# Optimization experiments

Hardware: AMD Instinct MI355X
Metric: run time of the kernel (lower is better)

Reference implementation:

```python
import jax, jax.numpy as jnp
import numpy as np

F_DIM = 4096
HID = 256
COR = 32
N_FRAMES = 200
NB = 30
TS = 9  # 4 + 5 time_steps


def _gru(xg, hg, wx, wh, bx, bh):
    # torch.nn.GRU cell math, gates ordered (r, z, n)
    gx = xg @ wx + bx
    gh = hg @ wh + bh
    xr, xz, xn = jnp.split(gx, 3, axis=-1)
    hr, hz, hn = jnp.split(gh, 3, axis=-1)
    r = jax.nn.sigmoid(xr + hr)
    z = jax.nn.sigmoid(xz + hz)
    n = jnp.tanh(xn + r * hn)
    return (1.0 - z) * n + z * hg


def _sattn(h, mask):
    # parameter-free scaled dot-product attention across active tracks
    d = jnp.asarray(h.shape[-1], h.dtype)
    s = (h @ h.T) / jnp.sqrt(d)
    s = jnp.where(mask[None, :], s, -1e9)
    a = jax.nn.softmax(s, axis=-1)
    out = a @ h
    return jnp.where(mask[:, None], out, h)


def setup_inputs() -> dict:
    key = jax.random.key(0)
    ks = jax.random.split(key, 20)
    flow = jax.random.normal(ks[0], (1, N_FRAMES, NB + 1, F_DIM), jnp.float32)
    x = jax.random.normal(ks[1], (1, N_FRAMES, NB + 1, F_DIM), jnp.float32)
    # y: [track_id, x1,y1,x2,y2, label, conf, d0..d5] -> 13 channels
    track = jnp.broadcast_to(jnp.arange(1, NB + 1, dtype=jnp.float32)[None, None, :, None], (1, N_FRAMES, NB, 1))
    coords = jax.random.uniform(ks[2], (1, N_FRAMES, NB, 4), jnp.float32, 0.0, 1000.0)
    label = jnp.round(jax.random.uniform(ks[3], (1, N_FRAMES, NB, 1), jnp.float32))
    conf = jax.random.uniform(ks[4], (1, N_FRAMES, NB, 1), jnp.float32)
    dist = jax.random.normal(ks[5], (1, N_FRAMES, NB, 6), jnp.float32)
    y = jnp.concatenate([track, coords, label, conf, dist], axis=-1)
    toa = jnp.ones((1, 1), jnp.float32)
    s = 0.02
    p = lambda k, shp: s * jax.random.normal(k, shp, jnp.float32)
    return {
        "x": x, "y": y, "toa": toa, "flow": flow,
        "W_rgb": p(ks[6], (F_DIM, HID)), "b_rgb": jnp.zeros((HID,), jnp.float32),
        "W_bb": p(ks[7], (5, HID)), "b_bb": jnp.zeros((HID,), jnp.float32),
        "W_dd": p(ks[8], (6, HID)), "b_dd": jnp.zeros((HID,), jnp.float32),
        "W_proj": p(ks[9], (HID, COR)), "b_proj": jnp.zeros((COR,), jnp.float32),
        "Wx_c": p(ks[10], (COR, 3 * COR)), "Wh_c": p(ks[11], (COR, 3 * COR)),
        "bx_c": jnp.zeros((3 * COR,), jnp.float32), "bh_c": jnp.zeros((3 * COR,), jnp.float32),
        "Wx_g": p(ks[12], (2 * HID, 3 * HID)), "Wh_g": p(ks[13], (HID, 3 * HID)),
        "bx_g": jnp.zeros((3 * HID,), jnp.float32), "bh_g": jnp.zeros((3 * HID,), jnp.float32),
        "W_out": p(ks[14], (2 * HID + COR, 1)), "b_out": jnp.zeros((1,), jnp.float32),
        "W_pbox": p(ks[15], (2 * HID + COR, 4 * TS)), "b_pbox": jnp.zeros((4 * TS,), jnp.float32),
    }


def reference(x, y, toa, flow, W_rgb, b_rgb, W_bb, b_bb, W_dd, b_dd, W_proj, b_proj,
              Wx_c, Wh_c, bx_c, bh_c, Wx_g, Wh_g, bx_g, bh_g, W_out, b_out, W_pbox, b_pbox):
    T = x.shape[1] - TS
    norm = jnp.array([1920.0, 1200.0, 1920.0, 1200.0], y.dtype)
    nb = y[0, :, :, 1:5] / norm                      # (N, 30, 4) normalized boxes
    # future targets: 9 future frames of normalized boxes, flattened -> (T, 30, 36)
    fut = jnp.concatenate([nb[1 + i:1 + i + T] for i in range(TS)], axis=-1)
    flow_f = flow[0, :T]                             # (T, 31, F)
    yf = y[0, :T]                                    # (T, 30, 13)
    nbf = nb[:T]
    act = yf[..., 0] != 0                            # (T, 30) active-track mask

    def step(carry, inp):
        h, hc, bacc, oacc = carry
        ft, yt, nbt, futt, at = inp
        atf = at.astype(h.dtype)
        rgb = jax.nn.relu(ft @ W_rgb + b_rgb)        # (31, H)
        img = jnp.broadcast_to(rgb[0], (NB, rgb.shape[-1]))
        comb = jnp.concatenate([rgb[1:], img], axis=-1)            # (30, 2H)
        bfeat = jax.nn.relu(jnp.concatenate([nbt, yt[:, 6:7]], axis=-1) @ W_bb + b_bb)
        dfeat = jax.nn.relu(yt[:, 7:13] @ W_dd + b_dd)
        xc = dfeat @ W_proj + b_proj
        hc_n = _gru(xc, hc, Wx_c, Wh_c, bx_c, bh_c)  # CorGRU, output_cor = hidden
        h_n = _gru(comb, h, Wx_g, Wh_g, bx_g, bh_g)
        feat = jnp.concatenate([h_n, bfeat, hc_n], axis=-1)        # (30, 2H+32)
        logit = (feat @ W_out + b_out)[:, 0]
        pbox = feat @ W_pbox + b_pbox                # (30, 36)
        d = pbox - futt
        ad = jnp.abs(d)
        sl1 = jnp.mean(jnp.where(ad < 1.0, 0.5 * d * d, ad - 0.5), axis=-1)  # SmoothL1 per box
        bacc = bacc + jnp.sum(sl1 * atf)
        tgt = yt[:, 5]
        bce = jnp.maximum(logit, 0.0) - logit * tgt + jnp.log1p(jnp.exp(-jnp.abs(logit)))
        oacc = oacc + 0.05 * jnp.sum(bce * atf)
        h2 = jnp.where(at[:, None], h_n, h)
        hc2 = jnp.where(at[:, None], hc_n, hc)
        return (_sattn(h2, at), _sattn(hc2, at), bacc, oacc), None

    init = (jnp.zeros((NB, HID), flow.dtype), jnp.zeros((NB, COR), flow.dtype),
            jnp.zeros((), flow.dtype), jnp.zeros((), flow.dtype))
    (h, hc, bbox_l, obj_l), _ = jax.lax.scan(step, init, (flow_f, yf, nbf, fut, act))
    total = obj_l + bbox_l + 0.3 * bbox_l            # object + bbox + inter(0.3*bbox)
    return total
```

## Files before the change

kernel.cpp:

```cpp
#include <hip/hip_runtime.h>
#include <hip/hip_bf16.h>
#include <math.h>
#include <stdint.h>

#define T_STEPS 191
#define NB1 31
#define YS 13

__device__ __forceinline__ float sigmoid_(float x) { return 1.f / (1.f + expf(-x)); }
__device__ __forceinline__ float bflo(unsigned u) { return __uint_as_float(u << 16); }
__device__ __forceinline__ float bfhi(unsigned u) { return __uint_as_float(u & 0xffff0000u); }

__device__ __forceinline__ void store_dw_mall(float* p, float v) {
    asm volatile("global_store_dword %0, %1, off sc0 sc1"
                 :: "v"((uintptr_t)p), "v"(v) : "memory");
}
__device__ __forceinline__ void atomic_inc_mall(unsigned* p) {
    asm volatile("global_atomic_add %0, %1, off sc1"
                 :: "v"((uintptr_t)p), "v"(1u) : "memory");
}
__device__ __forceinline__ unsigned load_u32_mall(const unsigned* p) {
    unsigned v;
    asm volatile("global_load_dword %0, %1, off sc0 sc1\n\ts_waitcnt vmcnt(0)"
                 : "=v"(v) : "v"((uintptr_t)p) : "memory");
    return v;
}

template <bool GATHER, bool RELU>
__global__ __launch_bounds__(256) void gemm_tiled(
    const float* __restrict__ A, const float* __restrict__ B,
    const float* __restrict__ bias, float* __restrict__ C,
    int M, int N, int K)
{
    __shared__ float As[16][65];
    __shared__ float Bs[16][65];
    const int tid = threadIdx.x;
    const int tm = tid >> 4, tn = tid & 15;
    const int rowBase = blockIdx.y * 64;
    const int colBase = blockIdx.x * 64;
    float acc[4][4] = {};
    for (int kt = 0; kt < K; kt += 16) {
        #pragma unroll
        for (int l = 0; l < 4; ++l) {
            const int idx = tid + l * 256;
            const int kk = idx & 15, rr = idx >> 4;
            const int row = rowBase + rr;
            float v = 0.f;
            if (row < M) {
                if (GATHER) {
                    const int t = row / 30, i = row - t * 30;
                    const int k = kt + kk;
                    const int src = (k < 256) ? ((t * NB1 + i + 1) * 256 + k)
                                              : (t * NB1 * 256 + (k - 256));
                    v = A[src];
                } else {
                    v = A[(size_t)row * K + kt + kk];
                }
            }
            As[kk][rr] = v;
            const int nn = idx & 63, k2 = idx >> 6;
            Bs[k2][nn] = B[(size_t)(kt + k2) * N + colBase + nn];
        }
        __syncthreads();
        #pragma unroll
        for (int kk = 0; kk < 16; ++kk) {
            float a[4], b[4];
            #pragma unroll
            for (int i = 0; i < 4; ++i) a[i] = As[kk][tm * 4 + i];
            #pragma unroll
            for (int j = 0; j < 4; ++j) b[j] = Bs[kk][tn * 4 + j];
            #pragma unroll
            for (int i = 0; i < 4; ++i)
                #pragma unroll
                for (int j = 0; j < 4; ++j)
                    acc[i][j] = fmaf(a[i], b[j], acc[i][j]);
        }
        __syncthreads();
    }
    #pragma unroll
    for (int i = 0; i < 4; ++i) {
        const int row = rowBase + tm * 4 + i;
        if (row < M) {
            #pragma unroll
            for (int j = 0; j < 4; ++j) {
                const int col = colBase + tn * 4 + j;
                float v = acc[i][j] + bias[col];
                if (RELU) v = fmaxf(v, 0.f);
                C[(size_t)row * N + col] = v;
            }
        }
    }
}

__global__ __launch_bounds__(256) void prep_w(const float* __restrict__ Whg, unsigned* __restrict__ wp)
{
    const int idx = blockIdx.x * 256 + threadIdx.x;
    if (idx >= 128 * 768) return;
    const int k2 = idx / 768, c = idx - k2 * 768;
    __hip_bfloat16 b0 = __float2bfloat16(Whg[(size_t)(2 * k2) * 768 + c]);
    __hip_bfloat16 b1 = __float2bfloat16(Whg[(size_t)(2 * k2 + 1) * 768 + c]);
    const unsigned lo = *reinterpret_cast<unsigned short*>(&b0);
    const unsigned hi = *reinterpret_cast<unsigned short*>(&b1);
    wp[idx] = lo | (hi << 16);
}

__global__ void prep_bias(const float* __restrict__ bxg, const float* __restrict__ bhg,
                          const float* __restrict__ bxc, const float* __restrict__ bhc,
                          float* __restrict__ biasg, float* __restrict__ biasc)
{
    const int t = threadIdx.x;
    if (t < 768) biasg[t] = bxg[t] + (t < 512 ? bhg[t] : 0.f);
    if (t < 96)  biasc[t] = bxc[t] + (t < 64 ? bhc[t] : 0.f);
}

__global__ __launch_bounds__(256) void precomp_kernel(
    const float* __restrict__ y,
    const float* __restrict__ Wbb, const float* __restrict__ bbb,
    const float* __restrict__ Wdd, const float* __restrict__ bdd,
    const float* __restrict__ Wproj, const float* __restrict__ bproj,
    const float* __restrict__ Wxc, const float* __restrict__ biasc,
    const float* __restrict__ Wpbox, const float* __restrict__ bpbox,
    const float* __restrict__ Wout, const float* __restrict__ bout,
    float* __restrict__ gxc, float* __restrict__ pbox_b, float* __restrict__ logit_b)
{
    const int m = blockIdx.x;
    const int tid = threadIdx.x;
    __shared__ float bf[256], df[256], xcs[32], yl[16];
    if (tid < YS) yl[tid] = y[m * YS + tid];
    __syncthreads();
    const float invnorm[4] = {1.f/1920.f, 1.f/1200.f, 1.f/1920.f, 1.f/1200.f};
    {
        float s = bbb[tid];
        s = fmaf(yl[1] * invnorm[0], Wbb[0 * 256 + tid], s);
        s = fmaf(yl[2] * invnorm[1], Wbb[1 * 256 + tid], s);
        s = fmaf(yl[3] * invnorm[2], Wbb[2 * 256 + tid], s);
        s = fmaf(yl[4] * invnorm[3], Wbb[3 * 256 + tid], s);
        s = fmaf(yl[6],              Wbb[4 * 256 + tid], s);
        bf[tid] = fmaxf(s, 0.f);
    }
    {
        float s = bdd[tid];
        #pragma unroll
        for (int k = 0; k < 6; ++k) s = fmaf(yl[7 + k], Wdd[k * 256 + tid], s);
        df[tid] = fmaxf(s, 0.f);
    }
    __syncthreads();
    {
        const int c = tid >> 3, p = tid & 7;
        float s = 0.f;
        for (int k = p; k < 256; k += 8) s = fmaf(df[k], Wproj[k * 32 + c], s);
        s += __shfl_xor(s, 1); s += __shfl_xor(s, 2); s += __shfl_xor(s, 4);
        if (p == 0) xcs[c] = s + bproj[c];
    }
    __syncthreads();
    if (tid < 96) {
        float s = biasc[tid];
        #pragma unroll
        for (int k = 0; k < 32; ++k) s = fmaf(xcs[k], Wxc[k * 96 + tid], s);
        gxc[m * 96 + tid] = s;
    }
    {
        const int d = tid >> 2, p = tid & 3;
        if (d < 37) {
            float s = 0.f;
            if (d < 36) {
                for (int k = p; k < 256; k += 4) s = fmaf(bf[k], Wpbox[(256 + k) * 36 + d], s);
            } else {
                for (int k = p; k < 256; k += 4) s = fmaf(bf[k], Wout[256 + k], s);
            }
            s += __shfl_xor(s, 1); s += __shfl_xor(s, 2);
            if (p == 0) {
                if (d < 36) pbox_b[m * 36 + d] = s + bpbox[d];
                else        logit_b[m] = s + bout[0];
            }
        }
    }
}

__device__ __forceinline__ void softmax30(const float* s, float* w) {
    float mx = -INFINITY;
    for (int j = 0; j < 30; ++j) mx = fmaxf(mx, s[j]);
    float sum = 0.f;
    for (int j = 0; j < 30; ++j) { const float e = expf(s[j] - mx); w[j] = e; sum += e; }
    const float inv = 1.f / sum;
    for (int j = 0; j < 30; ++j) w[j] *= inv;
}

#define PH 260
#define PC 36

__global__ __launch_bounds__(768) void seq_kernel(
    const float* __restrict__ y,
    const float* __restrict__ gxg,
    const float* __restrict__ gxc,
    const float* __restrict__ pbox_b,
    const float* __restrict__ logit_b,
    const unsigned* __restrict__ wp,
    const float* __restrict__ bhg,
    const float* __restrict__ Whc,
    const float* __restrict__ bhc,
    const float* __restrict__ Wpbox,
    const float* __restrict__ Wout,
    float* __restrict__ h2buf,
    float* __restrict__ hc2buf,
    unsigned* __restrict__ bar,
    float* __restrict__ partials)
{
    const int r = blockIdx.x;
    const int tid = threadIdx.x;
    __shared__ __align__(16) float h[256];
    __shared__ float gat[768];
    __shared__ float hn[256];
    __shared__ __align__(16) float h2l[256];
    __shared__ float hcs[32], hcg[96], hcn[32];
    __shared__ __align__(16) float hc2l[32];
    __shared__ float whc[32 * 96];
    __shared__ float sc[32], sc2[32], attw[32], attw2[32], pbl[40];
    __shared__ __align__(16) float h2s[30 * PH];
    __shared__ __align__(16) float hc2s[30 * PC];

    for (int i = tid; i < 32 * 96; i += 768) whc[i] = Whc[i];
    if (tid < 256) h[tid] = 0.f;
    if (tid < 32) hcs[tid] = 0.f;
    __syncthreads();

    float bacc = 0.f, oacc = 0.f;

    for (int t = 0; t < T_STEPS; ++t) {
        const int m = t * 30 + r;
        const bool act = (y[m * YS] != 0.f);
        const float actf = act ? 1.f : 0.f;
        const int buf = t & 1;
        float* hb  = h2buf  + buf * (30 * 256);
        float* hcb = hc2buf + buf * (30 * 32);

        {
            const unsigned* wc = wp + tid;
            const float4* h4 = (const float4*)h;
            float acc = 0.f;
            #pragma unroll 8
            for (int k2 = 0; k2 < 128; k2 += 2) {
                const float4 hv = h4[k2 >> 1];
                const unsigned w0 = wc[(size_t)k2 * 768];
                const unsigned w1 = wc[(size_t)(k2 + 1) * 768];
                acc = fmaf(hv.x, bflo(w0), acc);
                acc = fmaf(hv.y, bfhi(w0), acc);
                acc = fmaf(hv.z, bflo(w1), acc);
                acc = fmaf(hv.w, bfhi(w1), acc);
            }
            gat[tid] = acc + (tid < 512 ? gxg[(size_t)m * 768 + tid] : bhg[tid]);
        }
        if (tid < 96) {
            float a = (tid < 64) ? gxc[m * 96 + tid] : bhc[tid];
            #pragma unroll
            for (int k = 0; k < 32; ++k) a = fmaf(hcs[k], whc[k * 96 + tid], a);
            hcg[tid] = a;
        }
        __syncthreads();

        if (tid < 256) {
            const float rg = sigmoid_(gat[tid]);
            const float zg = sigmoid_(gat[256 + tid]);
            const float xn = gxg[(size_t)m * 768 + 512 + tid];
            const float ng = tanhf(xn + rg * gat[512 + tid]);
            const float hv = h[tid];
            const float hnv = (1.f - zg) * ng + zg * hv;
            hn[tid] = hnv;
            const float h2v = act ? hnv : hv;
            h2l[tid] = h2v;
            store_dw_mall(hb + r * 256 + tid, h2v);
        } else if (tid < 288) {
            const int j = tid - 256;
            const float rg = sigmoid_(hcg[j]);
            const float zg = sigmoid_(hcg[32 + j]);
            const float xn = gxc[m * 96 + 64 + j];
            const float ng = tanhf(xn + rg * hcg[64 + j]);
            const float hv = hcs[j];
            const float hvn = (1.f - zg) * ng + zg * hv;
            hcn[j] = hvn;
            const float h2v = act ? hvn : hv;
            hc2l[j] = h2v;
            store_dw_mall(hcb + r * 32 + j, h2v);
        }
        if (tid < 320) asm volatile("s_waitcnt vmcnt(0)" ::: "memory");
        __syncthreads();

        if (tid < 592) {
            const int d = tid >> 4, p = tid & 15;
            float s = 0.f;
            if (d < 36) {
                for (int k = p; k < 256; k += 16) s = fmaf(hn[k], Wpbox[k * 36 + d], s);
                for (int k = p; k < 32; k += 16)  s = fmaf(hcn[k], Wpbox[(512 + k) * 36 + d], s);
            } else {
                for (int k = p; k < 256; k += 16) s = fmaf(hn[k], Wout[k], s);
                for (int k = p; k < 32; k += 16)  s = fmaf(hcn[k], Wout[512 + k], s);
            }
            s += __shfl_xor(s, 1); s += __shfl_xor(s, 2); s += __shfl_xor(s, 4); s += __shfl_xor(s, 8);
            if (p == 0) pbl[d] = s + (d < 36 ? pbox_b[m * 36 + d] : logit_b[m]);
        }
        __syncthreads();

        if (tid < 64) {
            float term = 0.f;
            if (tid < 36) {
                const int s4 = tid >> 2, cc = tid & 3;
                const float fnorm = (cc & 1) ? (1.f / 1200.f) : (1.f / 1920.f);
                const float fut = y[((t + 1 + s4) * 30 + r) * YS + 1 + cc] * fnorm;
                const float d = pbl[tid] - fut;
                const float ad = fabsf(d);
                term = (ad < 1.f) ? 0.5f * d * d : (ad - 0.5f);
            }
            #pragma unroll
            for (int o = 1; o < 64; o <<= 1) term += __shfl_xor(term, o);
            if (tid == 0) {
                bacc += (term * (1.f / 36.f)) * actf;
                const float l = pbl[36];
                const float tgt = y[m * YS + 5];
                const float bce = fmaxf(l, 0.f) - l * tgt + log1pf(expf(-fabsf(l)));
                oacc += 0.05f * bce * actf;
                atomic_inc_mall(bar);
                const unsigned tgtc = 30u * (unsigned)(t + 1);
                unsigned cur;
                do {
                    asm volatile("s_sleep 1" :::);
                    cur = load_u32_mall(bar);
                } while (cur < tgtc);
            }
        }
        __syncthreads();

        {
            const int it0 = tid, it1 = tid + 768, it2 = tid + 1536;
            const float* s0; const float* s1; const float* s2;
            float* d0; float* d1; float* d2;
            {
                const int i = it0;
                s0 = hb + ((i >> 6) * 256 + (i & 63) * 4);
                d0 = &h2s[(i >> 6) * PH + (i & 63) * 4];
            }
            {
                const int i = it1;
                if (i < 1920) { s1 = hb + ((i >> 6) * 256 + (i & 63) * 4); d1 = &h2s[(i >> 6) * PH + (i & 63) * 4]; }
                else { const int i2 = i - 1920; s1 = hcb + ((i2 >> 3) * 32 + (i2 & 7) * 4); d1 = &hc2s[(i2 >> 3) * PC + (i2 & 7) * 4]; }
            }
            const bool has2 = (it2 < 2160);
            if (has2) {
                const int i = it2;
                if (i < 1920) { s2 = hb + ((i >> 6) * 256 + (i & 63) * 4); d2 = &h2s[(i >> 6) * PH + (i & 63) * 4]; }
                else { const int i2 = i - 1920; s2 = hcb + ((i2 >> 3) * 32 + (i2 & 7) * 4); d2 = &hc2s[(i2 >> 3) * PC + (i2 & 7) * 4]; }
            } else { s2 = s0; d2 = d0; }
            float4 v0, v1, v2;
            asm volatile("global_load_dwordx4 %0, %1, off sc0 sc1" : "=v"(v0) : "v"((uintptr_t)s0) : "memory");
            asm volatile("global_load_dwordx4 %0, %1, off sc0 sc1" : "=v"(v1) : "v"((uintptr_t)s1) : "memory");
            asm volatile("global_load_dwordx4 %0, %1, off sc0 sc1" : "=v"(v2) : "v"((uintptr_t)s2) : "memory");
            asm volatile("s_waitcnt vmcnt(0)" ::: "memory");
            *(float4*)d0 = v0;
            *(float4*)d1 = v1;
            if (has2) *(float4*)d2 = v2;
        }
        __syncthreads();

        if (tid < 480) {
            const int j = tid >> 4, p = tid & 15;
            float s = 0.f;
            for (int k = p; k < 256; k += 16) s = fmaf(h2l[k], h2s[j * PH + k], s);
            s += __shfl_xor(s, 1); s += __shfl_xor(s, 2); s += __shfl_xor(s, 4); s += __shfl_xor(s, 8);
            if (p == 0) {
                const bool actj = (y[(t * 30 + j) * YS] != 0.f);
                sc[j] = actj ? s * (1.f / 16.f) : -1e9f;
            }
        } else if (tid < 510) {
            const int j = tid - 480;
            float s = 0.f;
            #pragma unroll
            for (int k = 0; k < 32; ++k) s = fmaf(hc2l[k], hc2s[j * PC + k], s);
            const bool actj = (y[(t * 30 + j) * YS] != 0.f);
            sc2[j] = actj ? s * 0.17677669529663687f : -1e9f;
        }
        __syncthreads();
        if (tid == 0)       softmax30(sc,  attw);
        else if (tid == 64) softmax30(sc2, attw2);
        __syncthreads();
        if (tid < 256) {
            float nh = 0.f;
            #pragma unroll 6
            for (int j = 0; j < 30; ++j) nh = fmaf(attw[j], h2s[j * PH + tid], nh);
            h[tid] = act ? nh : h2l[tid];
        } else if (tid < 288) {
            const int j2 = tid - 256;
            float nc = 0.f;
            #pragma unroll
            for (int j = 0; j < 30; ++j) nc = fmaf(attw2[j], hc2s[j * PC + j2], nc);
            hcs[j2] = act ? nc : hc2l[j2];
        }
        __syncthreads();
    }

    if (tid == 0) { partials[r] = bacc; partials[30 + r] = oacc; }
}

__global__ void reduce_kernel(const float* __restrict__ partials, float* __restrict__ out) {
    if (threadIdx.x == 0) {
        float b = 0.f, o = 0.f;
        for (int i = 0; i < 30; ++i) { b += partials[i]; o += partials[30 + i]; }
        out[0] = o + b + 0.3f * b;
    }
}

extern "C" void kernel_launch(void* const* d_in, const int* in_sizes, int n_in,
                              void* d_out, int out_size, void* d_ws, size_t ws_size,
                              hipStream_t stream) {
    (void)in_sizes; (void)n_in; (void)out_size; (void)ws_size;
    const float* y      = (const float*)d_in[1];
    const float* flow   = (const float*)d_in[3];
    const float* W_rgb  = (const float*)d_in[4];
    const float* b_rgb  = (const float*)d_in[5];
    const float* W_bb   = (const float*)d_in[6];
    const float* b_bb   = (const float*)d_in[7];
    const float* W_dd   = (const float*)d_in[8];
    const float* b_dd   = (const float*)d_in[9];
    const float* W_proj = (const float*)d_in[10];
    const float* b_proj = (const float*)d_in[11];
    const float* Wx_c   = (const float*)d_in[12];
    const float* Wh_c   = (const float*)d_in[13];
    const float* bx_c   = (const float*)d_in[14];
    const float* bh_c   = (const float*)d_in[15];
    const float* Wx_g   = (const float*)d_in[16];
    const float* Wh_g   = (const float*)d_in[17];
    const float* bx_g   = (const float*)d_in[18];
    const float* bh_g   = (const float*)d_in[19];
    const float* W_out  = (const float*)d_in[20];
    const float* b_out  = (const float*)d_in[21];
    const float* W_pbox = (const float*)d_in[22];
    const float* b_pbox = (const float*)d_in[23];
    float* out = (float*)d_out;

    char* ws = (char*)d_ws;
    unsigned* bar = (unsigned*)ws;
    float* base = (float*)(ws + 256);
    size_t off = 0;
    float* rgb    = base + off; off += (size_t)5921 * 256;
    float* gxg    = base + off; off += (size_t)5730 * 768;
    float* gxc    = base + off; off += (size_t)5730 * 96;
    float* pboxb  = base + off; off += (size_t)5730 * 36;
    float* logitb = base + off; off += 5730;
    float* h2b    = base + off; off += 2 * 30 * 256;
    float* hc2b   = base + off; off += 2 * 30 * 32;
    float* parts  = base + off; off += 64;
    unsigned* wp  = (unsigned*)(base + off); off += 128 * 768;
    float* biasg  = base + off; off += 768;
    float* biasc  = base + off; off += 96;

    (void)hipMemsetAsync(d_ws, 0, 256, stream);

    prep_w<<<(128 * 768 + 255) / 256, 256, 0, stream>>>(Wh_g, wp);
    prep_bias<<<1, 768, 0, stream>>>(bx_g, bh_g, bx_c, bh_c, biasg, biasc);

    gemm_tiled<false, true><<<dim3(4, 93), 256, 0, stream>>>(flow, W_rgb, b_rgb, rgb, 5921, 256, 4096);
    gemm_tiled<true, false><<<dim3(12, 90), 256, 0, stream>>>(rgb, Wx_g, biasg, gxg, 5730, 768, 512);
    precomp_kernel<<<5730, 256, 0, stream>>>(y, W_bb, b_bb, W_dd, b_dd, W_proj, b_proj,
                                             Wx_c, biasc, W_pbox, b_pbox, W_out, b_out,
                                             gxc, pboxb, logitb);
    seq_kernel<<<30, 768, 0, stream>>>(y, gxg, gxc, pboxb, logitb, wp, bh_g, Wh_c, bh_c,
                                       W_pbox, W_out, h2b, hc2b, bar, parts);
    reduce_kernel<<<1, 64, 0, stream>>>(parts, out);
}
```

Measured before the change: 5.067 ms.

## Run the sequential GRU scan in one block with bf16 MFMA and split precision

The sequential recurrence no longer runs as 30 blocks (one per track) that meet at a spin barrier through global memory every step. It now runs in a single 512-thread block that handles all 30 tracks together. The hidden-state GEMMs, the output heads and the attention are done with 32x32x16 bf16 MFMA instructions, using hi/lo bf16 splitting to keep close to fp32 accuracy. New prep kernels pre-swizzle the weights into MFMA fragment layout, and the final reduction is folded into the kernel. This removes the cross-block barrier and global round-trips, at the cost of running on one CU with extra MFMA passes for precision.

```diff
diff --git a/kernel.cpp b/kernel.cpp
--- a/kernel.cpp
+++ b/kernel.cpp
@@ -1,5 +1,4 @@
 #include <hip/hip_runtime.h>
-#include <hip/hip_bf16.h>
 #include <math.h>
 #include <stdint.h>
 
@@ -7,23 +6,38 @@
 #define NB1 31
 #define YS 13
 
-__device__ __forceinline__ float sigmoid_(float x) { return 1.f / (1.f + expf(-x)); }
-__device__ __forceinline__ float bflo(unsigned u) { return __uint_as_float(u << 16); }
-__device__ __forceinline__ float bfhi(unsigned u) { return __uint_as_float(u & 0xffff0000u); }
-
-__device__ __forceinline__ void store_dw_mall(float* p, float v) {
-    asm volatile("global_store_dword %0, %1, off sc0 sc1"
-                 :: "v"((uintptr_t)p), "v"(v) : "memory");
-}
-__device__ __forceinline__ void atomic_inc_mall(unsigned* p) {
-    asm volatile("global_atomic_add %0, %1, off sc1"
-                 :: "v"((uintptr_t)p), "v"(1u) : "memory");
-}
-__device__ __forceinline__ unsigned load_u32_mall(const unsigned* p) {
-    unsigned v;
-    asm volatile("global_load_dword %0, %1, off sc0 sc1\n\ts_waitcnt vmcnt(0)"
-                 : "=v"(v) : "v"((uintptr_t)p) : "memory");
-    return v;
+typedef short bf8 __attribute__((ext_vector_type(8)));
+typedef float f16x __attribute__((ext_vector_type(16)));
+
+#define MFMA32 __builtin_amdgcn_mfma_f32_32x32x16_bf16
+
+__device__ __forceinline__ unsigned bf16b(float x){
+  unsigned u = __float_as_uint(x);
+  return (u + 0x7fffu + ((u>>16)&1u)) >> 16;
+}
+__device__ __forceinline__ float bf16f(unsigned b){ return __uint_as_float(b<<16); }
+
+__device__ __forceinline__ bf8 ldfrag(const unsigned short* p, int slot){
+  uint4 u = *reinterpret_cast<const uint4*>(p + slot*8);
+  return __builtin_bit_cast(bf8, u);
+}
+__device__ __forceinline__ bf8 ldg4(const unsigned* p){
+  uint4 u = *reinterpret_cast<const uint4*>(p);
+  return __builtin_bit_cast(bf8, u);
+}
+__device__ __forceinline__ bf8 gather8(const unsigned short* fr, int base){
+  unsigned w0 = (unsigned)fr[base]    | ((unsigned)fr[base+8]<<16);
+  unsigned w1 = (unsigned)fr[base+16] | ((unsigned)fr[base+24]<<16);
+  unsigned w2 = (unsigned)fr[base+32] | ((unsigned)fr[base+40]<<16);
+  unsigned w3 = (unsigned)fr[base+48] | ((unsigned)fr[base+56]<<16);
+  uint4 u; u.x=w0; u.y=w1; u.z=w2; u.w=w3;
+  return __builtin_bit_cast(bf8, u);
+}
+__device__ __forceinline__ f16x zf16(){
+  f16x v;
+#pragma unroll
+  for (int q=0;q<16;++q) v[q]=0.f;
+  return v;
 }
 
 template <bool GATHER, bool RELU>
@@ -92,16 +106,66 @@
     }
 }
 
-__global__ __launch_bounds__(256) void prep_w(const float* __restrict__ Whg, unsigned* __restrict__ wp)
+__global__ __launch_bounds__(256) void prep_wg(const float* __restrict__ Whg,
+                                               unsigned* __restrict__ wpg)
 {
     const int idx = blockIdx.x * 256 + threadIdx.x;
-    if (idx >= 128 * 768) return;
-    const int k2 = idx / 768, c = idx - k2 * 768;
-    __hip_bfloat16 b0 = __float2bfloat16(Whg[(size_t)(2 * k2) * 768 + c]);
-    __hip_bfloat16 b1 = __float2bfloat16(Whg[(size_t)(2 * k2 + 1) * 768 + c]);
-    const unsigned lo = *reinterpret_cast<unsigned short*>(&b0);
-    const unsigned hi = *reinterpret_cast<unsigned short*>(&b1);
-    wp[idx] = lo | (hi << 16);
+    const int j  = idx & 3;
+    const int l  = (idx >> 2) & 63;
+    const int kb = (idx >> 8) & 15;
+    const int nt = idx >> 12;
+    const int g = nt / 3, gate = nt - g * 3;
+    const int col = gate * 256 + g * 32 + (l & 31);
+    const int k2 = kb * 8 + ((l >> 5) << 2) + j;
+    const unsigned lo = bf16b(Whg[(size_t)(2 * k2) * 768 + col]);
+    const unsigned hi = bf16b(Whg[(size_t)(2 * k2 + 1) * 768 + col]);
+    wpg[idx] = lo | (hi << 16);
+}
+
+__global__ __launch_bounds__(256) void prep_hd(const float* __restrict__ Wpbox,
+                                               const float* __restrict__ Wout,
+                                               unsigned* __restrict__ hdh,
+                                               unsigned* __restrict__ hdl)
+{
+    const int idx = blockIdx.x * 256 + threadIdx.x;
+    if (idx >= 9216) return;
+    const int j = idx & 3;
+    const int l = (idx >> 2) & 63;
+    const int kbnt = idx >> 8;
+    const int kb = kbnt % 18, nt = kbnt / 18;
+    const int d = nt * 32 + (l & 31);
+    const int k0 = kb * 16 + ((l >> 5) << 3) + 2 * j;
+    float v0 = 0.f, v1 = 0.f;
+    if (d < 37) {
+        const int r0 = (k0 < 256) ? k0 : 512 + (k0 - 256);
+        const int r1 = (k0 + 1 < 256) ? (k0 + 1) : 512 + (k0 + 1 - 256);
+        v0 = (d < 36) ? Wpbox[(size_t)r0 * 36 + d] : Wout[r0];
+        v1 = (d < 36) ? Wpbox[(size_t)r1 * 36 + d] : Wout[r1];
+    }
+    const unsigned h0 = bf16b(v0), h1 = bf16b(v1);
+    const unsigned l0 = bf16b(v0 - bf16f(h0)), l1 = bf16b(v1 - bf16f(h1));
+    hdh[idx] = h0 | (h1 << 16);
+    hdl[idx] = l0 | (l1 << 16);
+}
+
+__global__ __launch_bounds__(256) void prep_hcw(const float* __restrict__ Whc,
+                                                unsigned* __restrict__ hch,
+                                                unsigned* __restrict__ hcl)
+{
+    const int idx = blockIdx.x * 256 + threadIdx.x;
+    if (idx >= 1536) return;
+    const int j = idx & 3;
+    const int l = (idx >> 2) & 63;
+    const int kb = (idx >> 8) & 1;
+    const int nt = idx >> 9;
+    const int col = nt * 32 + (l & 31);
+    const int k0 = kb * 16 + ((l >> 5) << 3) + 2 * j;
+    const float v0 = Whc[k0 * 96 + col];
+    const float v1 = Whc[(k0 + 1) * 96 + col];
+    const unsigned h0 = bf16b(v0), h1 = bf16b(v1);
+    const unsigned l0 = bf16b(v0 - bf16f(h0)), l1 = bf16b(v1 - bf16f(h1));
+    hch[idx] = h0 | (h1 << 16);
+    hcl[idx] = l0 | (l1 << 16);
 }
 
 __global__ void prep_bias(const float* __restrict__ bxg, const float* __restrict__ bhg,
@@ -177,233 +241,325 @@
     }
 }
 
-__device__ __forceinline__ void softmax30(const float* s, float* w) {
-    float mx = -INFINITY;
-    for (int j = 0; j < 30; ++j) mx = fmaxf(mx, s[j]);
-    float sum = 0.f;
-    for (int j = 0; j < 30; ++j) { const float e = expf(s[j] - mx); w[j] = e; sum += e; }
-    const float inv = 1.f / sum;
-    for (int j = 0; j < 30; ++j) w[j] *= inv;
-}
-
-#define PH 260
-#define PC 36
-
-__global__ __launch_bounds__(768) void seq_kernel(
+__global__ __launch_bounds__(512, 2) void seq2(
     const float* __restrict__ y,
     const float* __restrict__ gxg,
     const float* __restrict__ gxc,
     const float* __restrict__ pbox_b,
     const float* __restrict__ logit_b,
-    const unsigned* __restrict__ wp,
+    const unsigned* __restrict__ wpg,
+    const unsigned* __restrict__ hdh, const unsigned* __restrict__ hdl,
+    const unsigned* __restrict__ hch, const unsigned* __restrict__ hcl,
     const float* __restrict__ bhg,
-    const float* __restrict__ Whc,
     const float* __restrict__ bhc,
-    const float* __restrict__ Wpbox,
-    const float* __restrict__ Wout,
-    float* __restrict__ h2buf,
-    float* __restrict__ hc2buf,
-    unsigned* __restrict__ bar,
-    float* __restrict__ partials)
+    float* __restrict__ out)
 {
-    const int r = blockIdx.x;
     const int tid = threadIdx.x;
-    __shared__ __align__(16) float h[256];
-    __shared__ float gat[768];
-    __shared__ float hn[256];
-    __shared__ __align__(16) float h2l[256];
-    __shared__ float hcs[32], hcg[96], hcn[32];
-    __shared__ __align__(16) float hc2l[32];
-    __shared__ float whc[32 * 96];
-    __shared__ float sc[32], sc2[32], attw[32], attw2[32], pbl[40];
-    __shared__ __align__(16) float h2s[30 * PH];
-    __shared__ __align__(16) float hc2s[30 * PC];
-
-    for (int i = tid; i < 32 * 96; i += 768) whc[i] = Whc[i];
-    if (tid < 256) h[tid] = 0.f;
-    if (tid < 32) hcs[tid] = 0.f;
+    const int lane = tid & 63, wid = tid >> 6;
+    const int half = lane >> 5, ln31 = lane & 31;
+
+    __shared__ __align__(16) unsigned short hf_hi[16*64*8], hf_lo[16*64*8];
+    __shared__ __align__(16) unsigned short cf_hi[2*64*8],  cf_lo[2*64*8];
+    __shared__ __align__(16) unsigned short wf_hi[2*64*8],  wf_lo[2*64*8];
+    __shared__ float hcbuf[32*33];
+    __shared__ float wcs[32*33];
+    __shared__ float ssc[32*33];
+    __shared__ float pbl[32*40];
+    __shared__ float actf[32], bhn[256], bhcn[32], red[16];
+
+    for (int i = tid; i < 16*64*8; i += 512){ hf_hi[i]=0; hf_lo[i]=0; }
+    for (int i = tid; i < 2*64*8; i += 512){ cf_hi[i]=0; cf_lo[i]=0; wf_hi[i]=0; wf_lo[i]=0; }
+    for (int i = tid; i < 32*33; i += 512) hcbuf[i] = 0.f;
+    if (tid < 256) bhn[tid] = bhg[512 + tid];
+    if (tid < 32)  bhcn[tid] = bhc[64 + tid];
+
+    float hreg[16];
+#pragma unroll
+    for (int q = 0; q < 16; ++q) hreg[q] = 0.f;
+    float bacc = 0.f, oacc = 0.f;
     __syncthreads();
 
-    float bacc = 0.f, oacc = 0.f;
+    const int dd = (wid << 5) + ln31;
+    const float bnd = bhn[dd];
 
     for (int t = 0; t < T_STEPS; ++t) {
-        const int m = t * 30 + r;
-        const bool act = (y[m * YS] != 0.f);
-        const float actf = act ? 1.f : 0.f;
-        const int buf = t & 1;
-        float* hb  = h2buf  + buf * (30 * 256);
-        float* hcb = hc2buf + buf * (30 * 32);
-
+        const int m0 = t * 30;
+
+        float gr[16], gz[16], gn[16];
+#pragma unroll
+        for (int q = 0; q < 16; ++q) {
+            const int obj = (q&3) + ((q>>2)<<3) + (half<<2);
+            if (obj < 30) {
+                const float* gp = gxg + (size_t)(m0 + obj) * 768 + dd;
+                gr[q] = gp[0]; gz[q] = gp[256]; gn[q] = gp[512];
+            } else { gr[q] = 0.f; gz[q] = 0.f; gn[q] = 0.f; }
+        }
+        f16x cR = zf16(), cZ = zf16(), cN = zf16();
+        float gcr[16], gcz[16], gcn[16];
+        if (wid == 7) {
+#pragma unroll
+            for (int q = 0; q < 16; ++q) {
+                const int obj = (q&3) + ((q>>2)<<3) + (half<<2);
+                if (obj < 30) {
+                    const float* gp = gxc + (size_t)(m0 + obj) * 96 + ln31;
+                    gcr[q] = gp[0]; gcz[q] = gp[32]; gcn[q] = gp[64];
+                } else { gcr[q] = 0.f; gcz[q] = 0.f; gcn[q] = 0.f; }
+            }
+        }
+        if (tid < 32) actf[tid] = (tid < 30 && y[(size_t)(m0 + tid) * YS] != 0.f) ? 1.f : 0.f;
+
+        f16x aR = zf16(), aZ = zf16(), aN = zf16();
         {
-            const unsigned* wc = wp + tid;
-            const float4* h4 = (const float4*)h;
-            float acc = 0.f;
-            #pragma unroll 8
-            for (int k2 = 0; k2 < 128; k2 += 2) {
-                const float4 hv = h4[k2 >> 1];
-                const unsigned w0 = wc[(size_t)k2 * 768];
-                const unsigned w1 = wc[(size_t)(k2 + 1) * 768];
-                acc = fmaf(hv.x, bflo(w0), acc);
-                acc = fmaf(hv.y, bfhi(w0), acc);
-                acc = fmaf(hv.z, bflo(w1), acc);
-                acc = fmaf(hv.w, bfhi(w1), acc);
-            }
-            gat[tid] = acc + (tid < 512 ? gxg[(size_t)m * 768 + tid] : bhg[tid]);
-        }
-        if (tid < 96) {
-            float a = (tid < 64) ? gxc[m * 96 + tid] : bhc[tid];
-            #pragma unroll
-            for (int k = 0; k < 32; ++k) a = fmaf(hcs[k], whc[k * 96 + tid], a);
-            hcg[tid] = a;
-        }
-        __syncthreads();
-
-        if (tid < 256) {
-            const float rg = sigmoid_(gat[tid]);
-            const float zg = sigmoid_(gat[256 + tid]);
-            const float xn = gxg[(size_t)m * 768 + 512 + tid];
-            const float ng = tanhf(xn + rg * gat[512 + tid]);
-            const float hv = h[tid];
-            const float hnv = (1.f - zg) * ng + zg * hv;
-            hn[tid] = hnv;
-            const float h2v = act ? hnv : hv;
-            h2l[tid] = h2v;
-            store_dw_mall(hb + r * 256 + tid, h2v);
-        } else if (tid < 288) {
-            const int j = tid - 256;
-            const float rg = sigmoid_(hcg[j]);
-            const float zg = sigmoid_(hcg[32 + j]);
-            const float xn = gxc[m * 96 + 64 + j];
-            const float ng = tanhf(xn + rg * hcg[64 + j]);
-            const float hv = hcs[j];
-            const float hvn = (1.f - zg) * ng + zg * hv;
-            hcn[j] = hvn;
-            const float h2v = act ? hvn : hv;
-            hc2l[j] = h2v;
-            store_dw_mall(hcb + r * 32 + j, h2v);
-        }
-        if (tid < 320) asm volatile("s_waitcnt vmcnt(0)" ::: "memory");
-        __syncthreads();
-
-        if (tid < 592) {
-            const int d = tid >> 4, p = tid & 15;
-            float s = 0.f;
-            if (d < 36) {
-                for (int k = p; k < 256; k += 16) s = fmaf(hn[k], Wpbox[k * 36 + d], s);
-                for (int k = p; k < 32; k += 16)  s = fmaf(hcn[k], Wpbox[(512 + k) * 36 + d], s);
-            } else {
-                for (int k = p; k < 256; k += 16) s = fmaf(hn[k], Wout[k], s);
-                for (int k = p; k < 32; k += 16)  s = fmaf(hcn[k], Wout[512 + k], s);
-            }
-            s += __shfl_xor(s, 1); s += __shfl_xor(s, 2); s += __shfl_xor(s, 4); s += __shfl_xor(s, 8);
-            if (p == 0) pbl[d] = s + (d < 36 ? pbox_b[m * 36 + d] : logit_b[m]);
-        }
-        __syncthreads();
-
-        if (tid < 64) {
-            float term = 0.f;
-            if (tid < 36) {
-                const int s4 = tid >> 2, cc = tid & 3;
-                const float fnorm = (cc & 1) ? (1.f / 1200.f) : (1.f / 1920.f);
-                const float fut = y[((t + 1 + s4) * 30 + r) * YS + 1 + cc] * fnorm;
-                const float d = pbl[tid] - fut;
-                const float ad = fabsf(d);
-                term = (ad < 1.f) ? 0.5f * d * d : (ad - 0.5f);
-            }
-            #pragma unroll
-            for (int o = 1; o < 64; o <<= 1) term += __shfl_xor(term, o);
-            if (tid == 0) {
-                bacc += (term * (1.f / 36.f)) * actf;
-                const float l = pbl[36];
-                const float tgt = y[m * YS + 5];
-                const float bce = fmaxf(l, 0.f) - l * tgt + log1pf(expf(-fabsf(l)));
-                oacc += 0.05f * bce * actf;
-                atomic_inc_mall(bar);
-                const unsigned tgtc = 30u * (unsigned)(t + 1);
-                unsigned cur;
-                do {
-                    asm volatile("s_sleep 1" :::);
-                    cur = load_u32_mall(bar);
-                } while (cur < tgtc);
+            const unsigned* bRp = wpg + ((size_t)((wid*3 + 0)*16)*64 + lane)*4;
+            const unsigned* bZp = wpg + ((size_t)((wid*3 + 1)*16)*64 + lane)*4;
+            const unsigned* bNp = wpg + ((size_t)((wid*3 + 2)*16)*64 + lane)*4;
+#pragma unroll 4
+            for (int kb = 0; kb < 16; ++kb) {
+                const bf8 br = ldg4(bRp + kb*256);
+                const bf8 bz = ldg4(bZp + kb*256);
+                const bf8 bn = ldg4(bNp + kb*256);
+                const bf8 ah = ldfrag(hf_hi, kb*64 + lane);
+                const bf8 al = ldfrag(hf_lo, kb*64 + lane);
+                aR = MFMA32(ah, br, aR, 0,0,0); aR = MFMA32(al, br, aR, 0,0,0);
+                aZ = MFMA32(ah, bz, aZ, 0,0,0); aZ = MFMA32(al, bz, aZ, 0,0,0);
+                aN = MFMA32(ah, bn, aN, 0,0,0); aN = MFMA32(al, bn, aN, 0,0,0);
+            }
+        }
+        if (wid == 7) {
+#pragma unroll
+            for (int kb = 0; kb < 2; ++kb) {
+                const bf8 ah = ldfrag(cf_hi, kb*64 + lane);
+                const bf8 al = ldfrag(cf_lo, kb*64 + lane);
+                const bf8 r_h = ldg4(hch + ((0*2 + kb)*64 + lane)*4);
+                const bf8 r_l = ldg4(hcl + ((0*2 + kb)*64 + lane)*4);
+                const bf8 z_h = ldg4(hch + ((1*2 + kb)*64 + lane)*4);
+                const bf8 z_l = ldg4(hcl + ((1*2 + kb)*64 + lane)*4);
+                const bf8 n_h = ldg4(hch + ((2*2 + kb)*64 + lane)*4);
+                const bf8 n_l = ldg4(hcl + ((2*2 + kb)*64 + lane)*4);
+                cR = MFMA32(ah, r_h, cR, 0,0,0); cR = MFMA32(ah, r_l, cR, 0,0,0); cR = MFMA32(al, r_h, cR, 0,0,0);
+                cZ = MFMA32(ah, z_h, cZ, 0,0,0); cZ = MFMA32(ah, z_l, cZ, 0,0,0); cZ = MFMA32(al, z_h, cZ, 0,0,0);
+                cN = MFMA32(ah, n_h, cN, 0,0,0); cN = MFMA32(ah, n_l, cN, 0,0,0); cN = MFMA32(al, n_h, cN, 0,0,0);
+            }
+        }
+        __syncthreads();
+
+#pragma unroll
+        for (int q = 0; q < 16; ++q) {
+            const int obj = (q&3) + ((q>>2)<<3) + (half<<2);
+            const float hv = hreg[q];
+            const float r = 1.f / (1.f + expf(-(aR[q] + gr[q])));
+            const float z = 1.f / (1.f + expf(-(aZ[q] + gz[q])));
+            const float n = tanhf(gn[q] + r * (aN[q] + bnd));
+            const float hn2 = (1.f - z) * n + z * hv;
+            const float h2 = (actf[obj] > 0.f) ? hn2 : hv;
+            hreg[q] = h2;
+            const unsigned hb = bf16b(h2);
+            const unsigned lb = bf16b(h2 - bf16f(hb));
+            const int sl = ((dd>>4)*64 + obj + ((dd>>3)&1)*32)*8 + (dd&7);
+            hf_hi[sl] = (unsigned short)hb; hf_lo[sl] = (unsigned short)lb;
+        }
+        if (wid == 7) {
+            const float bnc = bhcn[ln31];
+#pragma unroll
+            for (int q = 0; q < 16; ++q) {
+                const int obj = (q&3) + ((q>>2)<<3) + (half<<2);
+                const float hcv = hcbuf[obj*33 + ln31];
+                const float r = 1.f / (1.f + expf(-(cR[q] + gcr[q])));
+                const float z = 1.f / (1.f + expf(-(cZ[q] + gcz[q])));
+                const float n = tanhf(gcn[q] + r * (cN[q] + bnc));
+                const float c2 = (actf[obj] > 0.f) ? (1.f - z) * n + z * hcv : hcv;
+                hcbuf[obj*33 + ln31] = c2;
+                const unsigned hb = bf16b(c2);
+                const unsigned lb = bf16b(c2 - bf16f(hb));
+                const int sl = ((ln31>>4)*64 + obj + ((ln31>>3)&1)*32)*8 + (ln31&7);
+                cf_hi[sl] = (unsigned short)hb; cf_lo[sl] = (unsigned short)lb;
+            }
+        }
+        __syncthreads();
+
+        if (wid == 0) {
+            f16x s1 = zf16(), s2 = zf16(), s3 = zf16();
+#pragma unroll 4
+            for (int kb = 0; kb < 16; ++kb) {
+                const bf8 ah = ldfrag(hf_hi, kb*64 + lane);
+                const bf8 al = ldfrag(hf_lo, kb*64 + lane);
+                s1 = MFMA32(ah, ah, s1, 0,0,0);
+                s2 = MFMA32(ah, al, s2, 0,0,0);
+                s3 = MFMA32(al, ah, s3, 0,0,0);
+            }
+#pragma unroll
+            for (int q = 0; q < 16; ++q) {
+                const int row = (q&3) + ((q>>2)<<3) + (half<<2);
+                const float sv = (s1[q] + s2[q] + s3[q]) * 0.0625f;
+                ssc[row*33 + ln31] = (actf[ln31] > 0.f) ? sv : -1e9f;
+            }
+        } else if (wid <= 2) {
+            const int nt = wid - 1;
+            f16x h1 = zf16(), h2v = zf16(), h3 = zf16();
+#pragma unroll 4
+            for (int kb = 0; kb < 16; ++kb) {
+                const bf8 ah = ldfrag(hf_hi, kb*64 + lane);
+                const bf8 al = ldfrag(hf_lo, kb*64 + lane);
+                const bf8 wh = ldg4(hdh + ((nt*18 + kb)*64 + lane)*4);
+                const bf8 wl = ldg4(hdl + ((nt*18 + kb)*64 + lane)*4);
+                h1 = MFMA32(ah, wh, h1, 0,0,0);
+                h2v = MFMA32(al, wh, h2v, 0,0,0);
+                h3 = MFMA32(ah, wl, h3, 0,0,0);
+            }
+#pragma unroll
+            for (int kb = 16; kb < 18; ++kb) {
+                const bf8 ah = ldfrag(cf_hi, (kb-16)*64 + lane);
+                const bf8 al = ldfrag(cf_lo, (kb-16)*64 + lane);
+                const bf8 wh = ldg4(hdh + ((nt*18 + kb)*64 + lane)*4);
+                const bf8 wl = ldg4(hdl + ((nt*18 + kb)*64 + lane)*4);
+                h1 = MFMA32(ah, wh, h1, 0,0,0);
+                h2v = MFMA32(al, wh, h2v, 0,0,0);
+                h3 = MFMA32(ah, wl, h3, 0,0,0);
+            }
+            const int d = nt*32 + ln31;
+            if (d < 37) {
+#pragma unroll
+                for (int q = 0; q < 16; ++q) {
+                    const int obj = (q&3) + ((q>>2)<<3) + (half<<2);
+                    pbl[obj*40 + d] = h1[q] + h2v[q] + h3[q];
+                }
+            }
+        } else if (wid <= 4) {
+            for (int ii = 0; ii < 15; ++ii) {
+                const int i = (wid - 3) * 15 + ii;
+                float ss = 0.f;
+#pragma unroll
+                for (int kk = 0; kk < 16; ++kk) {
+                    const int k = half*16 + kk;
+                    ss = fmaf(hcbuf[i*33 + k], hcbuf[ln31*33 + k], ss);
+                }
+                ss += __shfl_xor(ss, 32);
+                if (half == 0)
+                    wcs[i*33 + ln31] = (actf[ln31] > 0.f) ? ss * 0.17677669529663687f : -1e9f;
+            }
+        }
+        __syncthreads();
+
+        if (wid == 0) {
+            if (lane < 30) {
+                float mx = -1e30f;
+                for (int j2 = 0; j2 < 30; ++j2) mx = fmaxf(mx, ssc[lane*33 + j2]);
+                float sum = 0.f;
+                for (int j2 = 0; j2 < 30; ++j2) sum += expf(ssc[lane*33 + j2] - mx);
+                const float inv = 1.f / sum;
+                for (int j2 = 0; j2 < 32; ++j2) {
+                    const float w = (j2 < 30) ? expf(ssc[lane*33 + j2] - mx) * inv : 0.f;
+                    const unsigned hb = bf16b(w);
+                    const unsigned lb = bf16b(w - bf16f(hb));
+                    const int sl = ((j2>>4)*64 + lane + ((j2>>3)&1)*32)*8 + (j2&7);
+                    wf_hi[sl] = (unsigned short)hb; wf_lo[sl] = (unsigned short)lb;
+                }
+            }
+        } else if (wid == 1) {
+            if (lane < 30) {
+                float mx = -1e30f;
+                for (int j2 = 0; j2 < 30; ++j2) mx = fmaxf(mx, wcs[lane*33 + j2]);
+                float sum = 0.f;
+                for (int j2 = 0; j2 < 30; ++j2) sum += expf(wcs[lane*33 + j2] - mx);
+                const float inv = 1.f / sum;
+                for (int j2 = 0; j2 < 30; ++j2) {
+                    const float v = expf(wcs[lane*33 + j2] - mx) * inv;
+                    wcs[lane*33 + j2] = v;
+                }
+            }
+        } else {
+            const int c0 = tid - 128;
+#pragma unroll
+            for (int r3 = 0; r3 < 3; ++r3) {
+                const int c = c0 + 384 * r3;
+                if (c < 1110) {
+                    const int obj = c / 37, d = c - obj * 37;
+                    if (actf[obj] > 0.f) {
+                        const int m = m0 + obj;
+                        if (d < 36) {
+                            const int s4 = d >> 2, cc = d & 3;
+                            const float fn = (cc & 1) ? (1.f/1200.f) : (1.f/1920.f);
+                            const float fu = y[(size_t)((t + 1 + s4)*30 + obj)*YS + 1 + cc] * fn;
+                            const float df = pbl[obj*40 + d] + pbox_b[(size_t)m*36 + d] - fu;
+                            const float ad = fabsf(df);
+                            bacc += ((ad < 1.f) ? 0.5f*df*df : ad - 0.5f) * (1.f/36.f);
+                        } else {
+                            const float l = pbl[obj*40 + 36] + logit_b[m];
+                            const float tg = y[(size_t)m*YS + 5];
+                            oacc += 0.05f * (fmaxf(l, 0.f) - l*tg + log1pf(expf(-fabsf(l))));
+                        }
+                    }
+                }
             }
         }
         __syncthreads();
 
         {
-            const int it0 = tid, it1 = tid + 768, it2 = tid + 1536;
-            const float* s0; const float* s1; const float* s2;
-            float* d0; float* d1; float* d2;
-            {
-                const int i = it0;
-                s0 = hb + ((i >> 6) * 256 + (i & 63) * 4);
-                d0 = &h2s[(i >> 6) * PH + (i & 63) * 4];
-            }
-            {
-                const int i = it1;
-                if (i < 1920) { s1 = hb + ((i >> 6) * 256 + (i & 63) * 4); d1 = &h2s[(i >> 6) * PH + (i & 63) * 4]; }
-                else { const int i2 = i - 1920; s1 = hcb + ((i2 >> 3) * 32 + (i2 & 7) * 4); d1 = &hc2s[(i2 >> 3) * PC + (i2 & 7) * 4]; }
-            }
-            const bool has2 = (it2 < 2160);
-            if (has2) {
-                const int i = it2;
-                if (i < 1920) { s2 = hb + ((i >> 6) * 256 + (i & 63) * 4); d2 = &h2s[(i >> 6) * PH + (i & 63) * 4]; }
-                else { const int i2 = i - 1920; s2 = hcb + ((i2 >> 3) * 32 + (i2 & 7) * 4); d2 = &hc2s[(i2 >> 3) * PC + (i2 & 7) * 4]; }
-            } else { s2 = s0; d2 = d0; }
-            float4 v0, v1, v2;
-            asm volatile("global_load_dwordx4 %0, %1, off sc0 sc1" : "=v"(v0) : "v"((uintptr_t)s0) : "memory");
-            asm volatile("global_load_dwordx4 %0, %1, off sc0 sc1" : "=v"(v1) : "v"((uintptr_t)s1) : "memory");
-            asm volatile("global_load_dwordx4 %0, %1, off sc0 sc1" : "=v"(v2) : "v"((uintptr_t)s2) : "memory");
-            asm volatile("s_waitcnt vmcnt(0)" ::: "memory");
-            *(float4*)d0 = v0;
-            *(float4*)d1 = v1;
-            if (has2) *(float4*)d2 = v2;
-        }
-        __syncthreads();
-
-        if (tid < 480) {
-            const int j = tid >> 4, p = tid & 15;
-            float s = 0.f;
-            for (int k = p; k < 256; k += 16) s = fmaf(h2l[k], h2s[j * PH + k], s);
-            s += __shfl_xor(s, 1); s += __shfl_xor(s, 2); s += __shfl_xor(s, 4); s += __shfl_xor(s, 8);
-            if (p == 0) {
-                const bool actj = (y[(t * 30 + j) * YS] != 0.f);
-                sc[j] = actj ? s * (1.f / 16.f) : -1e9f;
-            }
-        } else if (tid < 510) {
-            const int j = tid - 480;
-            float s = 0.f;
-            #pragma unroll
-            for (int k = 0; k < 32; ++k) s = fmaf(hc2l[k], hc2s[j * PC + k], s);
-            const bool actj = (y[(t * 30 + j) * YS] != 0.f);
-            sc2[j] = actj ? s * 0.17677669529663687f : -1e9f;
-        }
-        __syncthreads();
-        if (tid == 0)       softmax30(sc,  attw);
-        else if (tid == 64) softmax30(sc2, attw2);
-        __syncthreads();
-        if (tid < 256) {
-            float nh = 0.f;
-            #pragma unroll 6
-            for (int j = 0; j < 30; ++j) nh = fmaf(attw[j], h2s[j * PH + tid], nh);
-            h[tid] = act ? nh : h2l[tid];
-        } else if (tid < 288) {
-            const int j2 = tid - 256;
-            float nc = 0.f;
-            #pragma unroll
-            for (int j = 0; j < 30; ++j) nc = fmaf(attw2[j], hc2s[j * PC + j2], nc);
-            hcs[j2] = act ? nc : hc2l[j2];
-        }
-        __syncthreads();
-    }
-
-    if (tid == 0) { partials[r] = bacc; partials[30 + r] = oacc; }
-}
-
-__global__ void reduce_kernel(const float* __restrict__ partials, float* __restrict__ out) {
-    if (threadIdx.x == 0) {
+            f16x ao = zf16();
+#pragma unroll
+            for (int kb2 = 0; kb2 < 2; ++kb2) {
+                const bf8 wh = ldfrag(wf_hi, kb2*64 + lane);
+                const bf8 wl = ldfrag(wf_lo, kb2*64 + lane);
+                const int base = ((dd>>4)*64 + kb2*16 + (half<<3) + ((dd>>3)&1)*32)*8 + (dd&7);
+                const bf8 bh = gather8(hf_hi, base);
+                const bf8 bl = gather8(hf_lo, base);
+                ao = MFMA32(wh, bh, ao, 0,0,0);
+                ao = MFMA32(wh, bl, ao, 0,0,0);
+                ao = MFMA32(wl, bh, ao, 0,0,0);
+            }
+#pragma unroll
+            for (int q = 0; q < 16; ++q) {
+                const int obj = (q&3) + ((q>>2)<<3) + (half<<2);
+                hreg[q] = (actf[obj] > 0.f) ? ao[q] : hreg[q];
+            }
+        }
+        float hcnew[8];
+        if (wid >= 6) {
+#pragma unroll
+            for (int qq = 0; qq < 8; ++qq) {
+                const int q = qq + ((wid - 6) << 3);
+                const int i = (q&3) + ((q>>2)<<3) + (half<<2);
+                float a2 = 0.f;
+                for (int j2 = 0; j2 < 30; ++j2)
+                    a2 = fmaf(wcs[i*33 + j2], hcbuf[j2*33 + ln31], a2);
+                hcnew[qq] = (actf[i] > 0.f) ? a2 : hcbuf[i*33 + ln31];
+            }
+        }
+        __syncthreads();
+
+#pragma unroll
+        for (int q = 0; q < 16; ++q) {
+            const int obj = (q&3) + ((q>>2)<<3) + (half<<2);
+            const float v = hreg[q];
+            const unsigned hb = bf16b(v);
+            const unsigned lb = bf16b(v - bf16f(hb));
+            const int sl = ((dd>>4)*64 + obj + ((dd>>3)&1)*32)*8 + (dd&7);
+            hf_hi[sl] = (unsigned short)hb; hf_lo[sl] = (unsigned short)lb;
+        }
+        if (wid >= 6) {
+#pragma unroll
+            for (int qq = 0; qq < 8; ++qq) {
+                const int q = qq + ((wid - 6) << 3);
+                const int i = (q&3) + ((q>>2)<<3) + (half<<2);
+                const float v = hcnew[qq];
+                hcbuf[i*33 + ln31] = v;
+                const unsigned hb = bf16b(v);
+                const unsigned lb = bf16b(v - bf16f(hb));
+                const int sl = ((ln31>>4)*64 + i + ((ln31>>3)&1)*32)*8 + (ln31&7);
+                cf_hi[sl] = (unsigned short)hb; cf_lo[sl] = (unsigned short)lb;
+            }
+        }
+        __syncthreads();
+    }
+
+#pragma unroll
+    for (int o = 1; o < 64; o <<= 1) { bacc += __shfl_xor(bacc, o); oacc += __shfl_xor(oacc, o); }
+    if (lane == 0) { red[wid] = bacc; red[8 + wid] = oacc; }
+    __syncthreads();
+    if (tid == 0) {
         float b = 0.f, o = 0.f;
-        for (int i = 0; i < 30; ++i) { b += partials[i]; o += partials[30 + i]; }
-        out[0] = o + b + 0.3f * b;
+        for (int i2 = 0; i2 < 8; ++i2) { b += red[i2]; o += red[8 + i2]; }
+        out[0] = o + 1.3f * b;
     }
 }
 
@@ -435,33 +591,31 @@
     const float* b_pbox = (const float*)d_in[23];
     float* out = (float*)d_out;
 
-    char* ws = (char*)d_ws;
-    unsigned* bar = (unsigned*)ws;
-    float* base = (float*)(ws + 256);
+    float* base = (float*)d_ws;
     size_t off = 0;
     float* rgb    = base + off; off += (size_t)5921 * 256;
     float* gxg    = base + off; off += (size_t)5730 * 768;
     float* gxc    = base + off; off += (size_t)5730 * 96;
     float* pboxb  = base + off; off += (size_t)5730 * 36;
-    float* logitb = base + off; off += 5730;
-    float* h2b    = base + off; off += 2 * 30 * 256;
-    float* hc2b   = base + off; off += 2 * 30 * 32;
-    float* parts  = base + off; off += 64;
-    unsigned* wp  = (unsigned*)(base + off); off += 128 * 768;
+    float* logitb = base + off; off += 5760;
     float* biasg  = base + off; off += 768;
     float* biasc  = base + off; off += 96;
-
-    (void)hipMemsetAsync(d_ws, 0, 256, stream);
-
-    prep_w<<<(128 * 768 + 255) / 256, 256, 0, stream>>>(Wh_g, wp);
+    unsigned* wpg = (unsigned*)(base + off); off += 98304;
+    unsigned* hdh = (unsigned*)(base + off); off += 9216;
+    unsigned* hdl = (unsigned*)(base + off); off += 9216;
+    unsigned* hch = (unsigned*)(base + off); off += 1536;
+    unsigned* hcl = (unsigned*)(base + off); off += 1536;
+
     prep_bias<<<1, 768, 0, stream>>>(bx_g, bh_g, bx_c, bh_c, biasg, biasc);
+    prep_wg<<<384, 256, 0, stream>>>(Wh_g, wpg);
+    prep_hd<<<36, 256, 0, stream>>>(W_pbox, W_out, hdh, hdl);
+    prep_hcw<<<6, 256, 0, stream>>>(Wh_c, hch, hcl);
 
     gemm_tiled<false, true><<<dim3(4, 93), 256, 0, stream>>>(flow, W_rgb, b_rgb, rgb, 5921, 256, 4096);
     gemm_tiled<true, false><<<dim3(12, 90), 256, 0, stream>>>(rgb, Wx_g, biasg, gxg, 5730, 768, 512);
     precomp_kernel<<<5730, 256, 0, stream>>>(y, W_bb, b_bb, W_dd, b_dd, W_proj, b_proj,
                                              Wx_c, biasc, W_pbox, b_pbox, W_out, b_out,
                                              gxc, pboxb, logitb);
-    seq_kernel<<<30, 768, 0, stream>>>(y, gxg, gxc, pboxb, logitb, wp, bh_g, Wh_c, bh_c,
-                                       W_pbox, W_out, h2b, hc2b, bar, parts);
-    reduce_kernel<<<1, 64, 0, stream>>>(parts, out);
-}
+    seq2<<<1, 512, 0, stream>>>(y, gxg, gxc, pboxb, logitb, wpg, hdh, hdl, hch, hcl,
+                                bh_g, bh_c, out);
+}
```

After: 11.17 ms. 121% more time.
